# Optimization experiments

Hardware: AMD Instinct MI355X
Metric: run time of the kernel (lower is better)

## Reference

```python
import jax, jax.numpy as jnp
import numpy as np

N_EMBD = 2048
NUM_GROUPS = 8
EXPERTS_PER_GROUP = 8
ROUTER_TEMPERATURE = 1.0
N_TOKENS = 16384


def setup_inputs() -> dict:
    key = jax.random.key(0)
    kx, kg, ke = jax.random.split(key, 3)
    x = jax.random.normal(kx, (N_TOKENS, N_EMBD), dtype=jnp.float32)
    # nn.Linear(in, out, bias=False) stores weight as [out, in]; kaiming-uniform-ish scale
    bound = 1.0 / np.sqrt(N_EMBD)
    group_gate_w = jax.random.uniform(kg, (NUM_GROUPS, N_EMBD), dtype=jnp.float32,
                                      minval=-bound, maxval=bound)
    expert_gate_w = jax.random.uniform(ke, (NUM_GROUPS * EXPERTS_PER_GROUP, N_EMBD),
                                       dtype=jnp.float32, minval=-bound, maxval=bound)
    return {"x": x, "group_gate_w": group_gate_w, "expert_gate_w": expert_gate_w}


def reference(x, group_gate_w, expert_gate_w):
    N = x.shape[0]
    G = NUM_GROUPS
    E_g = EXPERTS_PER_GROUP
    inv_temp = 1.0 / ROUTER_TEMPERATURE

    # Level 1: group routing
    group_logits = jnp.einsum('nd,gd->ng', x, group_gate_w)            # [N, G]
    group_probs = jax.nn.softmax(group_logits * inv_temp, axis=-1)     # [N, G]
    group_mask = group_probs >= (1.0 / G)                              # [N, G]

    # Level 2: expert routing within each group
    expert_logits = jnp.einsum('nd,ed->ne', x, expert_gate_w)          # [N, G*E_g]
    expert_logits = expert_logits.reshape(N, G, E_g)
    expert_probs = jax.nn.softmax(expert_logits * inv_temp, axis=-1)   # [N, G, E_g]
    expert_mask = expert_probs >= (1.0 / E_g)                          # [N, G, E_g]

    valid_mask_3d = group_mask[:, :, None] & expert_mask               # [N, G, E_g]
    selected_weights_3d = (group_probs[:, :, None] * expert_probs) * valid_mask_3d.astype(x.dtype)

    valid_mask = valid_mask_3d.reshape(N, G * E_g)
    selected_weights = selected_weights_3d.reshape(N, G * E_g)
    weight_sum = jnp.clip(jnp.sum(selected_weights, axis=-1, keepdims=True), 1e-9, None)
    normalized_weights = selected_weights / weight_sum
    return (valid_mask, normalized_weights)
```

## Files before the change

### kernel.cpp

```cpp
#include <hip/hip_runtime.h>


#define NT 16384
#define NE 2048
#define NTH 512
#define NBLK 256
#define NCHUNK 32
#define WCH 20480
#define LDS_BYTES 74752

typedef _Float16 v8h __attribute__((ext_vector_type(8)));
typedef float    v4f __attribute__((ext_vector_type(4)));

__global__ __launch_bounds__(256, 1)
void prep(const float* __restrict__ gw, const float* __restrict__ ew,
          _Float16* __restrict__ wf)
{
    const int t = blockIdx.x * 256 + threadIdx.x;
    const int j    = t & 7;
    const int sl   = (t >> 3) & 63;
    const int rest = t >> 9;
    const int g    = rest % 5;
    const int ks   = rest / 5;
    const int m = sl & 15, q = sl >> 4;
    const int gate = g * 16 + m;
    const int k = ks * 32 + q * 8 + j;
    float v = 0.f;
    if (gate < 64)      v = ew[gate * NE + k];
    else if (gate < 72) v = gw[(gate - 64) * NE + k];
    const _Float16 h = (_Float16)v;
    const int o = (((ks * 5 + g) * 2) * 64 + sl) * 8 + j;
    wf[o]       = h;
    wf[o + 512] = (_Float16)((v - (float)h) * 2048.0f);
}

__global__ __launch_bounds__(NTH, 2)
void router(const float* __restrict__ x, const _Float16* __restrict__ wf,
            float* __restrict__ out)
{
    __shared__ __align__(16) char sm[LDS_BYTES];
    const int tid  = threadIdx.x;
    const int lane = tid & 63;
    const int w    = tid >> 6;
    const int tt   = w >> 1, s2 = w & 1;
    const int t0   = blockIdx.x * 64;

    const float* xq = x + (size_t)(t0 + tt * 16 + (lane & 15)) * NE
                    + s2 * 32 + (lane >> 4) * 8;

    uint4 wr0, wr1, wr2;
    auto wload = [&](int c) {
        const char* src = (const char*)wf + (size_t)c * WCH;
        wr0 = *(const uint4*)(src + (0 * 512 + tid) * 16);
        wr1 = *(const uint4*)(src + (1 * 512 + tid) * 16);
        if (tid < 256) wr2 = *(const uint4*)(src + (1024 + tid) * 16);
    };
    auto wcommit = [&](int buf) {
        char* dst = sm + buf * WCH;
        *(uint4*)(dst + (0 * 512 + tid) * 16) = wr0;
        *(uint4*)(dst + (1 * 512 + tid) * 16) = wr1;
        if (tid < 256) *(uint4*)(dst + (1024 + tid) * 16) = wr2;
    };

    v4f accH[5], accC[5];
    #pragma unroll
    for (int g = 0; g < 5; ++g) { accH[g] = (v4f)(0.f); accC[g] = (v4f)(0.f); }

    const int wrd = s2 * 10240 + lane * 16;

    auto xload_to = [&](int c, float4& r0, float4& r1) {
        const float* p = xq + c * 64;
        r0 = *(const float4*)(p);
        r1 = *(const float4*)(p + 4);
    };

    auto mfma_block = [&](int P, const v8h& Bh, const v8h& Bl) {
        const char* wb = sm + P * WCH;
        #pragma unroll
        for (int g = 0; g < 5; ++g) {
            const char* wpg = wb + wrd + g * 2048;
            const v8h Ah = *(const v8h*)(wpg);
            const v8h Al = *(const v8h*)(wpg + 1024);
            accH[g] = __builtin_amdgcn_mfma_f32_16x16x32_f16(Ah, Bh, accH[g], 0, 0, 0);
            accC[g] = __builtin_amdgcn_mfma_f32_16x16x32_f16(Ah, Bl, accC[g], 0, 0, 0);
            accC[g] = __builtin_amdgcn_mfma_f32_16x16x32_f16(Al, Bh, accC[g], 0, 0, 0);
        }
    };

    auto step = [&](int c, int P, float4& cur0, float4& cur1) {
        __syncthreads();
        if (c + 1 < NCHUNK) wload(c + 1);
        v8h Bh, Bl;
        {
            const float v[8] = {cur0.x, cur0.y, cur0.z, cur0.w,
                                cur1.x, cur1.y, cur1.z, cur1.w};
            #pragma unroll
            for (int j = 0; j < 8; ++j) {
                const _Float16 hh = (_Float16)v[j];
                Bh[j] = hh;
                Bl[j] = (_Float16)((v[j] - (float)hh) * 2048.0f);
            }
        }
        if (c + 2 < NCHUNK) xload_to(c + 2, cur0, cur1);
        mfma_block(P, Bh, Bl);
        if (c + 1 < NCHUNK) wcommit(1 - P);
    };

    float4 xA0, xA1, xB0, xB1;

    wload(0);
    xload_to(0, xA0, xA1);
    xload_to(1, xB0, xB1);
    wcommit(0);

    #pragma unroll 1
    for (int cc = 0; cc < NCHUNK; cc += 2) {
        step(cc,     0, xA0, xA1);
        step(cc + 1, 1, xB0, xB1);
    }
    __syncthreads();

    float part[5][4];
    #pragma unroll
    for (int g = 0; g < 5; ++g)
        #pragma unroll
        for (int r = 0; r < 4; ++r)
            part[g][r] = accH[g][r] + accC[g][r] * (1.0f / 2048.0f);

    float* red = (float*)sm;
    if (s2 == 1) {
        #pragma unroll
        for (int g = 0; g < 5; ++g)
            #pragma unroll
            for (int r = 0; r < 4; ++r)
                red[((tt * 5 + g) * 4 + r) * 64 + lane] = part[g][r];
    }
    __syncthreads();
    float* la = (float*)(sm + 20480);
    if (s2 == 0) {
        #pragma unroll
        for (int g = 0; g < 5; ++g)
            #pragma unroll
            for (int r = 0; r < 4; ++r) {
                const float v = part[g][r] + red[((tt * 5 + g) * 4 + r) * 64 + lane];
                const int gate  = g * 16 + (lane >> 4) * 4 + r;
                const int token = tt * 16 + (lane & 15);
                la[token * 84 + gate] = v;
            }
    }
    __syncthreads();

    if (lane < 8) {
        const int token = w * 8 + lane;
        const float* lg = la + token * 84;
        float* M  = (float*)(sm + 41984) + token * 64;
        float* Wn = (float*)(sm + 58368) + token * 64;

        float gpb[8];
        float gmax = lg[64];
        #pragma unroll
        for (int g = 1; g < 8; ++g) gmax = fmaxf(gmax, lg[64 + g]);
        float gsum = 0.f;
        #pragma unroll
        for (int g = 0; g < 8; ++g) { gpb[g] = __expf(lg[64 + g] - gmax); gsum += gpb[g]; }
        const float ginv = 1.f / gsum;

        float sel[64];
        float wsum = 0.f;
        #pragma unroll
        for (int g = 0; g < 8; ++g) {
            const float gp_ = gpb[g] * ginv;
            float emax = lg[g * 8];
            #pragma unroll
            for (int j = 1; j < 8; ++j) emax = fmaxf(emax, lg[g * 8 + j]);
            float ep[8]; float esum = 0.f;
            #pragma unroll
            for (int j = 0; j < 8; ++j) { ep[j] = __expf(lg[g * 8 + j] - emax); esum += ep[j]; }
            const float einv = 1.f / esum;
            const bool gm = gp_ >= 0.125f;
            #pragma unroll
            for (int j = 0; j < 8; ++j) {
                const float pe = ep[j] * einv;
                const bool v = gm && (pe >= 0.125f);
                const float ww = v ? gp_ * pe : 0.f;
                M[g * 8 + j] = v ? 1.f : 0.f;
                sel[g * 8 + j] = ww;
                wsum += ww;
            }
        }
        const float inv = 1.f / fmaxf(wsum, 1e-9f);
        #pragma unroll
        for (int e = 0; e < 64; ++e) Wn[e] = sel[e] * inv;
    }
    __syncthreads();

    const float4* M4 = (const float4*)(sm + 41984);
    const float4* W4 = (const float4*)(sm + 58368);
    float4* o0 = (float4*)(out + (size_t)t0 * 64);
    float4* o1 = (float4*)(out + (size_t)NT * 64 + (size_t)t0 * 64);
    o0[tid]       = M4[tid];
    o0[tid + 512] = M4[tid + 512];
    o1[tid]       = W4[tid];
    o1[tid + 512] = W4[tid + 512];
}

extern "C" void kernel_launch(void* const* d_in, const int* in_sizes, int n_in,
                              void* d_out, int out_size, void* d_ws, size_t ws_size,
                              hipStream_t stream) {
    const float* x  = (const float*)d_in[0];
    const float* gw = (const float*)d_in[1];
    const float* ew = (const float*)d_in[2];
    float* out = (float*)d_out;
    _Float16* wf = (_Float16*)d_ws;
    (void)ws_size; (void)in_sizes; (void)n_in; (void)out_size;

    prep<<<dim3(640), dim3(256), 0, stream>>>(gw, ew, wf);
    router<<<dim3(NBLK), dim3(NTH), 0, stream>>>(x, wf, out);
}
```

Measured before the change: 210.9 us.

## Use direct global-to-LDS weight loads with four K-split waves and two token tiles

Each block now has 256 threads and handles 32 tokens, giving 512 blocks instead of 256. Each of the four waves owns one K-slice and computes two 16-token tiles, so every weight fragment read from LDS feeds twice as many MFMAs. Weight staging now uses global_load_lds async copies instead of a round trip through registers. The cost is a four-way cross-wave reduction of partial logits through LDS, plus a larger per-block LDS footprint that could limit occupancy.

```diff
diff --git a/kernel.cpp b/kernel.cpp
--- a/kernel.cpp
+++ b/kernel.cpp
@@ -3,11 +3,12 @@
 
 #define NT 16384
 #define NE 2048
-#define NTH 512
-#define NBLK 256
-#define NCHUNK 32
-#define WCH 20480
-#define LDS_BYTES 74752
+#define NTH 256
+#define NBLK 512
+#define NCHUNK 16
+#define KSB 10240
+#define WCH 40960
+#define LDS_BYTES 81920
 
 typedef _Float16 v8h __attribute__((ext_vector_type(8)));
 typedef float    v4f __attribute__((ext_vector_type(4)));
@@ -42,119 +43,124 @@
     const int tid  = threadIdx.x;
     const int lane = tid & 63;
     const int w    = tid >> 6;
-    const int tt   = w >> 1, s2 = w & 1;
-    const int t0   = blockIdx.x * 64;
-
-    const float* xq = x + (size_t)(t0 + tt * 16 + (lane & 15)) * NE
-                    + s2 * 32 + (lane >> 4) * 8;
-
-    uint4 wr0, wr1, wr2;
-    auto wload = [&](int c) {
-        const char* src = (const char*)wf + (size_t)c * WCH;
-        wr0 = *(const uint4*)(src + (0 * 512 + tid) * 16);
-        wr1 = *(const uint4*)(src + (1 * 512 + tid) * 16);
-        if (tid < 256) wr2 = *(const uint4*)(src + (1024 + tid) * 16);
-    };
-    auto wcommit = [&](int buf) {
-        char* dst = sm + buf * WCH;
-        *(uint4*)(dst + (0 * 512 + tid) * 16) = wr0;
-        *(uint4*)(dst + (1 * 512 + tid) * 16) = wr1;
-        if (tid < 256) *(uint4*)(dst + (1024 + tid) * 16) = wr2;
-    };
-
-    v4f accH[5], accC[5];
+    const int t0   = blockIdx.x * 32;
+
+    const float* xq0 = x + (size_t)(t0 + (lane & 15)) * NE + w * 32 + (lane >> 4) * 8;
+    const float* xq1 = xq0 + (size_t)16 * NE;
+
+    auto stage = [&](int c, int buf) {
+        const char* src = (const char*)wf + (size_t)c * WCH + w * KSB + lane * 16;
+        char* dst = sm + buf * WCH + w * KSB;
+        #pragma unroll
+        for (int i = 0; i < 10; ++i)
+            __builtin_amdgcn_global_load_lds(
+                (const __attribute__((address_space(1))) char*)(src + i * 1024),
+                (__attribute__((address_space(3))) char*)(dst + i * 1024),
+                16, 0, 0);
+    };
+
+    auto split8 = [](const float4& a, const float4& b, v8h& h, v8h& l) {
+        const float v[8] = {a.x, a.y, a.z, a.w, b.x, b.y, b.z, b.w};
+        #pragma unroll
+        for (int j = 0; j < 8; ++j) {
+            const _Float16 hh = (_Float16)v[j];
+            h[j] = hh;
+            l[j] = (_Float16)((v[j] - (float)hh) * 2048.0f);
+        }
+    };
+
+    v4f accH0[5], accC0[5], accH1[5], accC1[5];
     #pragma unroll
-    for (int g = 0; g < 5; ++g) { accH[g] = (v4f)(0.f); accC[g] = (v4f)(0.f); }
-
-    const int wrd = s2 * 10240 + lane * 16;
-
-    auto xload_to = [&](int c, float4& r0, float4& r1) {
-        const float* p = xq + c * 64;
-        r0 = *(const float4*)(p);
-        r1 = *(const float4*)(p + 4);
-    };
-
-    auto mfma_block = [&](int P, const v8h& Bh, const v8h& Bl) {
-        const char* wb = sm + P * WCH;
+    for (int g = 0; g < 5; ++g) {
+        accH0[g] = (v4f)(0.f); accC0[g] = (v4f)(0.f);
+        accH1[g] = (v4f)(0.f); accC1[g] = (v4f)(0.f);
+    }
+
+    auto xload = [&](int c, float4& a0, float4& a1, float4& b0, float4& b1) {
+        const float* p0 = xq0 + c * 128;
+        const float* p1 = xq1 + c * 128;
+        a0 = *(const float4*)(p0); a1 = *(const float4*)(p0 + 4);
+        b0 = *(const float4*)(p1); b1 = *(const float4*)(p1 + 4);
+    };
+
+    auto step = [&](int c, int P, float4& c00, float4& c01, float4& c10, float4& c11) {
+        __syncthreads();
+        if (c + 1 < NCHUNK) stage(c + 1, 1 - P);
+        v8h Bh0, Bl0, Bh1, Bl1;
+        split8(c00, c01, Bh0, Bl0);
+        split8(c10, c11, Bh1, Bl1);
+        if (c + 2 < NCHUNK) xload(c + 2, c00, c01, c10, c11);
+        const char* wb = sm + P * WCH + w * KSB + lane * 16;
         #pragma unroll
         for (int g = 0; g < 5; ++g) {
-            const char* wpg = wb + wrd + g * 2048;
-            const v8h Ah = *(const v8h*)(wpg);
-            const v8h Al = *(const v8h*)(wpg + 1024);
-            accH[g] = __builtin_amdgcn_mfma_f32_16x16x32_f16(Ah, Bh, accH[g], 0, 0, 0);
-            accC[g] = __builtin_amdgcn_mfma_f32_16x16x32_f16(Ah, Bl, accC[g], 0, 0, 0);
-            accC[g] = __builtin_amdgcn_mfma_f32_16x16x32_f16(Al, Bh, accC[g], 0, 0, 0);
-        }
-    };
-
-    auto step = [&](int c, int P, float4& cur0, float4& cur1) {
-        __syncthreads();
-        if (c + 1 < NCHUNK) wload(c + 1);
-        v8h Bh, Bl;
-        {
-            const float v[8] = {cur0.x, cur0.y, cur0.z, cur0.w,
-                                cur1.x, cur1.y, cur1.z, cur1.w};
-            #pragma unroll
-            for (int j = 0; j < 8; ++j) {
-                const _Float16 hh = (_Float16)v[j];
-                Bh[j] = hh;
-                Bl[j] = (_Float16)((v[j] - (float)hh) * 2048.0f);
-            }
-        }
-        if (c + 2 < NCHUNK) xload_to(c + 2, cur0, cur1);
-        mfma_block(P, Bh, Bl);
-        if (c + 1 < NCHUNK) wcommit(1 - P);
-    };
-
-    float4 xA0, xA1, xB0, xB1;
-
-    wload(0);
-    xload_to(0, xA0, xA1);
-    xload_to(1, xB0, xB1);
-    wcommit(0);
+            const v8h Ah = *(const v8h*)(wb + g * 2048);
+            const v8h Al = *(const v8h*)(wb + g * 2048 + 1024);
+            accH0[g] = __builtin_amdgcn_mfma_f32_16x16x32_f16(Ah, Bh0, accH0[g], 0, 0, 0);
+            accC0[g] = __builtin_amdgcn_mfma_f32_16x16x32_f16(Ah, Bl0, accC0[g], 0, 0, 0);
+            accC0[g] = __builtin_amdgcn_mfma_f32_16x16x32_f16(Al, Bh0, accC0[g], 0, 0, 0);
+            accH1[g] = __builtin_amdgcn_mfma_f32_16x16x32_f16(Ah, Bh1, accH1[g], 0, 0, 0);
+            accC1[g] = __builtin_amdgcn_mfma_f32_16x16x32_f16(Ah, Bl1, accC1[g], 0, 0, 0);
+            accC1[g] = __builtin_amdgcn_mfma_f32_16x16x32_f16(Al, Bh1, accC1[g], 0, 0, 0);
+        }
+    };
+
+    float4 xA00, xA01, xA10, xA11, xB00, xB01, xB10, xB11;
+
+    stage(0, 0);
+    xload(0, xA00, xA01, xA10, xA11);
+    xload(1, xB00, xB01, xB10, xB11);
 
     #pragma unroll 1
     for (int cc = 0; cc < NCHUNK; cc += 2) {
-        step(cc,     0, xA0, xA1);
-        step(cc + 1, 1, xB0, xB1);
-    }
-    __syncthreads();
-
-    float part[5][4];
+        step(cc,     0, xA00, xA01, xA10, xA11);
+        step(cc + 1, 1, xB00, xB01, xB10, xB11);
+    }
+    __syncthreads();
+
+    float part[2][5][4];
     #pragma unroll
     for (int g = 0; g < 5; ++g)
         #pragma unroll
-        for (int r = 0; r < 4; ++r)
-            part[g][r] = accH[g][r] + accC[g][r] * (1.0f / 2048.0f);
+        for (int r = 0; r < 4; ++r) {
+            part[0][g][r] = accH0[g][r] + accC0[g][r] * (1.0f / 2048.0f);
+            part[1][g][r] = accH1[g][r] + accC1[g][r] * (1.0f / 2048.0f);
+        }
 
     float* red = (float*)sm;
-    if (s2 == 1) {
-        #pragma unroll
-        for (int g = 0; g < 5; ++g)
-            #pragma unroll
-            for (int r = 0; r < 4; ++r)
-                red[((tt * 5 + g) * 4 + r) * 64 + lane] = part[g][r];
-    }
-    __syncthreads();
-    float* la = (float*)(sm + 20480);
-    if (s2 == 0) {
-        #pragma unroll
-        for (int g = 0; g < 5; ++g)
-            #pragma unroll
-            for (int r = 0; r < 4; ++r) {
-                const float v = part[g][r] + red[((tt * 5 + g) * 4 + r) * 64 + lane];
-                const int gate  = g * 16 + (lane >> 4) * 4 + r;
-                const int token = tt * 16 + (lane & 15);
-                la[token * 84 + gate] = v;
-            }
+    if (w > 0) {
+        #pragma unroll
+        for (int t = 0; t < 2; ++t)
+            #pragma unroll
+            for (int g = 0; g < 5; ++g)
+                #pragma unroll
+                for (int r = 0; r < 4; ++r)
+                    red[((((w - 1) * 2 + t) * 5 + g) * 4 + r) * 64 + lane] = part[t][g][r];
+    }
+    __syncthreads();
+    float* la = (float*)(sm + 30720);
+    if (w == 0) {
+        #pragma unroll
+        for (int t = 0; t < 2; ++t)
+            #pragma unroll
+            for (int g = 0; g < 5; ++g)
+                #pragma unroll
+                for (int r = 0; r < 4; ++r) {
+                    const float v = part[t][g][r]
+                        + red[(((0 * 2 + t) * 5 + g) * 4 + r) * 64 + lane]
+                        + red[(((1 * 2 + t) * 5 + g) * 4 + r) * 64 + lane]
+                        + red[(((2 * 2 + t) * 5 + g) * 4 + r) * 64 + lane];
+                    const int gate  = g * 16 + (lane >> 4) * 4 + r;
+                    const int token = t * 16 + (lane & 15);
+                    la[token * 84 + gate] = v;
+                }
     }
     __syncthreads();
 
     if (lane < 8) {
         const int token = w * 8 + lane;
         const float* lg = la + token * 84;
-        float* M  = (float*)(sm + 41984) + token * 64;
-        float* Wn = (float*)(sm + 58368) + token * 64;
+        float* M  = (float*)(sm + 41472) + token * 64;
+        float* Wn = (float*)(sm + 49664) + token * 64;
 
         float gpb[8];
         float gmax = lg[64];
@@ -194,14 +200,14 @@
     }
     __syncthreads();
 
-    const float4* M4 = (const float4*)(sm + 41984);
-    const float4* W4 = (const float4*)(sm + 58368);
+    const float4* M4 = (const float4*)(sm + 41472);
+    const float4* W4 = (const float4*)(sm + 49664);
     float4* o0 = (float4*)(out + (size_t)t0 * 64);
     float4* o1 = (float4*)(out + (size_t)NT * 64 + (size_t)t0 * 64);
     o0[tid]       = M4[tid];
-    o0[tid + 512] = M4[tid + 512];
+    o0[tid + 256] = M4[tid + 256];
     o1[tid]       = W4[tid];
-    o1[tid + 512] = W4[tid + 512];
+    o1[tid + 256] = W4[tid + 256];
 }
 
 extern "C" void kernel_launch(void* const* d_in, const int* in_sizes, int n_in,
```

New measurement: 205.5 us. -2.6%, faster.
